# Optimization experiments

Hardware: AMD Instinct MI355X
Metric: run time of the kernel (lower is better)

The kernel has to match this reference:

```python
import jax, jax.numpy as jnp
import numpy as np

H = 1024   # hidden_size
E = 8      # num_experts
B = 8192   # num tokens


def setup_inputs() -> dict:
    key = jax.random.key(0)
    ks = jax.random.split(key, 7)
    s = 1.0 / np.sqrt(H)
    return {
        "inputs": jax.random.normal(ks[0], (B, H), jnp.float32),
        "Wr": jax.random.uniform(ks[1], (H, E), jnp.float32, -s, s),
        "br": jax.random.uniform(ks[2], (E,), jnp.float32, -s, s),
        "W1": jax.random.uniform(ks[3], (E, H, H), jnp.float32, -s, s),
        "b1": jax.random.uniform(ks[4], (E, H), jnp.float32, -s, s),
        "W2": jax.random.uniform(ks[5], (E, H, H), jnp.float32, -s, s),
        "b2": jax.random.uniform(ks[6], (E, H), jnp.float32, -s, s),
        "top_k": 2,
    }


def reference(inputs, Wr, br, W1, b1, W2, b2, top_k):
    # Router: softmax over experts
    logits = inputs @ Wr + br                      # [B, E]
    weights = jax.nn.softmax(logits, axis=-1)      # [B, E]

    # Top-k mask + renormalize (matches scatter_ mask semantics)
    top_values, top_indices = jax.lax.top_k(weights, top_k)  # [B, k]
    rows = jnp.arange(weights.shape[0])[:, None]
    mask = jnp.zeros_like(weights).at[rows, top_indices].set(1.0)
    masked = weights * mask
    masked = masked / (masked.sum(axis=-1, keepdims=True) + 1e-9)

    # Dense all-experts MLP: Linear -> GELU(exact) -> Linear
    h = jnp.einsum('bh,ehf->bef', inputs, W1) + b1            # [B, E, H]
    h = jax.nn.gelu(h, approximate=False)
    expert_out = jnp.einsum('bef,efh->beh', h, W2) + b2       # [B, E, H]

    combined = jnp.einsum('be,beh->bh', masked, expert_out)   # [B, H]
    return combined, weights
```

## Files before the change

kernel.cpp:

```cpp
#include <hip/hip_runtime.h>
#include <math.h>


#define HB 1024
#define NB 8192
#define NE 8
#define RTOK 16

#define BM 128
#define BN 128
#define BK 64

typedef unsigned short ushort_t;
typedef unsigned int u32;
typedef _Float16 f16;
typedef __attribute__((ext_vector_type(8))) _Float16 hfx8;
typedef __attribute__((ext_vector_type(4))) float f32x4;

__device__ __forceinline__ float gelu_exact(float x) {
  return 0.5f * x * (1.0f + erff(x * 0.70710678118654752440f));
}
__device__ __forceinline__ void gload16(const void* g, void* l) {
  __builtin_amdgcn_global_load_lds((const __attribute__((address_space(1))) u32*)g,
                                   (__attribute__((address_space(3))) u32*)l, 16, 0, 0);
}

__global__ void zero_cnt_kernel(int* cnt) {
  if (threadIdx.x < NE * 16) cnt[threadIdx.x] = 0;
}

__global__ __launch_bounds__(256) void zero_out_kernel(float4* __restrict__ out) {
  out[(size_t)blockIdx.x * 256 + threadIdx.x] = (float4){0.f, 0.f, 0.f, 0.f};
}

__global__ __launch_bounds__(256) void xsplit_kernel(
    const float* __restrict__ X, f16* __restrict__ Xh, f16* __restrict__ Xl)
{
  const size_t i = ((size_t)blockIdx.x * 256 + threadIdx.x) * 8;
  float4 a = *(const float4*)(X + i);
  float4 b = *(const float4*)(X + i + 4);
  float f[8] = {a.x, a.y, a.z, a.w, b.x, b.y, b.z, b.w};
  hfx8 h, l;
  #pragma unroll
  for (int q = 0; q < 8; ++q) {
    f16 hh = (f16)f[q];
    h[q] = hh;
    l[q] = (f16)(f[q] - (float)hh);
  }
  *(hfx8*)(Xh + i) = h;
  *(hfx8*)(Xl + i) = l;
}

__global__ __launch_bounds__(256) void wsplit_kernel(
    const float* __restrict__ W1, const float* __restrict__ W2,
    f16* __restrict__ T1h, f16* __restrict__ T2h)
{
  __shared__ float sT[32][33];
  const int e = blockIdx.z >> 1;
  const int which = blockIdx.z & 1;
  const float* W = (which ? W2 : W1) + ((size_t)e << 20);
  f16* Th = (which ? T2h : T1h) + ((size_t)e << 20);
  const int k0 = blockIdx.x << 5;
  const int n0 = blockIdx.y << 5;
  const int r = threadIdx.x >> 3;
  const int q = threadIdx.x & 7;
  float4 v = *(const float4*)(W + (size_t)(k0 + r) * HB + n0 + q * 4);
  sT[r][q*4+0] = v.x; sT[r][q*4+1] = v.y; sT[r][q*4+2] = v.z; sT[r][q*4+3] = v.w;
  __syncthreads();
  f16 hv[4];
  #pragma unroll
  for (int j = 0; j < 4; ++j) hv[j] = (f16)sT[q*4+j][r];
  const size_t off = (size_t)(n0 + r) * HB + k0 + q * 4;
  *(ushort4*)(Th + off) = *(ushort4*)hv;
}

__global__ __launch_bounds__(256) void router_kernel(
    const float* __restrict__ X, const float* __restrict__ Wr, const float* __restrict__ br,
    float* __restrict__ wout, int* __restrict__ cnt,
    int* __restrict__ list, float* __restrict__ wlist)
{
  __shared__ int   sCnt[NE];
  __shared__ int   sBase[NE];
  __shared__ int   sE[RTOK][2];
  __shared__ int   sOff[RTOK][2];
  __shared__ float sW[RTOK][2];

  const int tid = threadIdx.x;
  if (tid < NE) sCnt[tid] = 0;
  __syncthreads();

  const int wv = tid >> 6;
  const int lane = tid & 63;

  for (int i = 0; i < 4; ++i) {
    const int s = wv * 4 + i;
    const int t = blockIdx.x * RTOK + s;
    const float* xr = X + (size_t)t * HB;
    float p0=0,p1=0,p2=0,p3=0,p4=0,p5=0,p6=0,p7=0;
    for (int h0 = 0; h0 < HB; h0 += 64) {
      float xv = xr[h0 + lane];
      const float4 wa = *(const float4*)(Wr + (size_t)(h0 + lane) * NE);
      const float4 wb = *(const float4*)(Wr + (size_t)(h0 + lane) * NE + 4);
      p0 += xv * wa.x; p1 += xv * wa.y; p2 += xv * wa.z; p3 += xv * wa.w;
      p4 += xv * wb.x; p5 += xv * wb.y; p6 += xv * wb.z; p7 += xv * wb.w;
    }
    #pragma unroll
    for (int off = 1; off < 64; off <<= 1) {
      p0 += __shfl_xor(p0, off); p1 += __shfl_xor(p1, off);
      p2 += __shfl_xor(p2, off); p3 += __shfl_xor(p3, off);
      p4 += __shfl_xor(p4, off); p5 += __shfl_xor(p5, off);
      p6 += __shfl_xor(p6, off); p7 += __shfl_xor(p7, off);
    }
    if (lane == 0) {
      float w[8];
      w[0]=p0+br[0]; w[1]=p1+br[1]; w[2]=p2+br[2]; w[3]=p3+br[3];
      w[4]=p4+br[4]; w[5]=p5+br[5]; w[6]=p6+br[6]; w[7]=p7+br[7];
      float m = w[0];
      #pragma unroll
      for (int e = 1; e < 8; ++e) m = fmaxf(m, w[e]);
      float sm = 0.f;
      #pragma unroll
      for (int e = 0; e < 8; ++e) { w[e] = expf(w[e] - m); sm += w[e]; }
      const float inv = 1.f / sm;
      #pragma unroll
      for (int e = 0; e < 8; ++e) w[e] *= inv;
      float4 w03; w03.x=w[0]; w03.y=w[1]; w03.z=w[2]; w03.w=w[3];
      float4 w47; w47.x=w[4]; w47.y=w[5]; w47.z=w[6]; w47.w=w[7];
      *(float4*)(wout + (size_t)t * NE)     = w03;
      *(float4*)(wout + (size_t)t * NE + 4) = w47;
      int i0 = 0; float v0 = w[0];
      #pragma unroll
      for (int e = 1; e < 8; ++e) if (w[e] > v0) { v0 = w[e]; i0 = e; }
      int i1 = -1; float v1 = -1.f;
      #pragma unroll
      for (int e = 0; e < 8; ++e) if (e != i0 && w[e] > v1) { v1 = w[e]; i1 = e; }
      const float rn = 1.f / (v0 + v1 + 1e-9f);
      const int o0 = atomicAdd(&sCnt[i0], 1);
      const int o1 = atomicAdd(&sCnt[i1], 1);
      sE[s][0] = i0; sOff[s][0] = o0; sW[s][0] = v0 * rn;
      sE[s][1] = i1; sOff[s][1] = o1; sW[s][1] = v1 * rn;
    }
  }
  __syncthreads();
  if (tid < NE) sBase[tid] = atomicAdd(&cnt[tid * 16], sCnt[tid]);
  __syncthreads();
  if (tid < RTOK * 2) {
    const int s = tid >> 1, j = tid & 1;
    const int t = blockIdx.x * RTOK + s;
    const int e = sE[s][j];
    const int pos = sBase[e] + sOff[s][j];
    list[e * NB + pos]  = t * 2 + j;
    wlist[e * NB + pos] = sW[s][j];
  }
}

__global__ __launch_bounds__(256, 3) void gemm1_kernel(
    const f16* __restrict__ Xh, const f16* __restrict__ Xl,
    const f16* __restrict__ Wh,
    const float* __restrict__ b1, const int* __restrict__ cnt, const int* __restrict__ list,
    f16* __restrict__ H1h, f16* __restrict__ H1l)
{
  const int e = blockIdx.z;
  const int ne = cnt[e << 4];
  const int m0 = blockIdx.x * BM;
  if (m0 >= ne) return;
  const int n0 = blockIdx.y * BN;

  __shared__ f16 sAh[BM][BK], sAl[BM][BK], sB[BN][BK];
  __shared__ int sId[BM];

  const int tid = threadIdx.x;
  if (tid < BM) {
    int idx = m0 + tid;
    sId[tid] = (idx < ne) ? list[e * NB + idx] : -1;
  }
  __syncthreads();

  const int lane = tid & 63;
  const int w    = tid >> 6;
  const int rl    = lane >> 3;
  const int xslot = (lane & 7) ^ rl;

  const f16* srcAh[4]; const f16* srcAl[4]; const f16* srcB[4];
  f16* dAh[4]; f16* dAl[4]; f16* dB[4];
  #pragma unroll
  for (int c = 0; c < 4; ++c) {
    const int cr = w * 32 + c * 8 + rl;
    const int rid = sId[cr];
    const size_t tok = (size_t)(rid < 0 ? 0 : (rid >> 1));
    srcAh[c] = Xh + (tok << 10) + xslot * 8;
    srcAl[c] = Xl + (tok << 10) + xslot * 8;
    const size_t nr = (size_t)(n0 + cr);
    srcB[c]  = Wh + ((size_t)e << 20) + (nr << 10) + xslot * 8;
    dAh[c] = &sAh[w * 32 + c * 8][0];
    dAl[c] = &sAl[w * 32 + c * 8][0];
    dB[c]  = &sB [w * 32 + c * 8][0];
  }

  const int wr = w >> 1, wc = w & 1;
  const int lrow = lane & 15;
  const int sgrp = lane >> 4;
  const int xk   = lrow & 7;

  f32x4 acc[4][4];
  #pragma unroll
  for (int i = 0; i < 4; ++i)
    #pragma unroll
    for (int j = 0; j < 4; ++j) acc[i][j] = (f32x4){0.f, 0.f, 0.f, 0.f};

  for (int k0 = 0; k0 < HB; k0 += BK) {
    #pragma unroll
    for (int c = 0; c < 4; ++c) {
      gload16(srcAh[c] + k0, dAh[c]);
      gload16(srcAl[c] + k0, dAl[c]);
      gload16(srcB[c]  + k0, dB[c]);
    }
    __syncthreads();
    #pragma unroll
    for (int ks = 0; ks < 2; ++ks) {
      const int col = ((ks * 4 + sgrp) ^ xk) * 8;
      hfx8 ah[4], al[4], b[4];
      #pragma unroll
      for (int m = 0; m < 4; ++m) {
        const int row = wr * 64 + m * 16 + lrow;
        ah[m] = *(const hfx8*)&sAh[row][col];
        al[m] = *(const hfx8*)&sAl[row][col];
      }
      #pragma unroll
      for (int n = 0; n < 4; ++n) {
        const int row = wc * 64 + n * 16 + lrow;
        b[n] = *(const hfx8*)&sB[row][col];
      }
      #pragma unroll
      for (int m = 0; m < 4; ++m)
        #pragma unroll
        for (int n = 0; n < 4; ++n) {
          acc[m][n] = __builtin_amdgcn_mfma_f32_16x16x32_f16(ah[m], b[n], acc[m][n], 0, 0, 0);
          acc[m][n] = __builtin_amdgcn_mfma_f32_16x16x32_f16(al[m], b[n], acc[m][n], 0, 0, 0);
        }
    }
    __syncthreads();
  }

  const int rgrp = (lane >> 4) << 2;
  #pragma unroll
  for (int m = 0; m < 4; ++m)
    #pragma unroll
    for (int r = 0; r < 4; ++r) {
      const int row = wr * 64 + m * 16 + rgrp + r;
      const int orid = sId[row];
      if (orid < 0) continue;
      #pragma unroll
      for (int n = 0; n < 4; ++n) {
        const int col = n0 + wc * 64 + n * 16 + lrow;
        float v = acc[m][n][r] + b1[e * HB + col];
        v = gelu_exact(v);
        f16 h = (f16)v;
        H1h[(size_t)orid * HB + col] = h;
        H1l[(size_t)orid * HB + col] = (f16)(v - (float)h);
      }
    }
}

__global__ __launch_bounds__(256, 3) void gemm2_kernel(
    const f16* __restrict__ H1h, const f16* __restrict__ H1l,
    const f16* __restrict__ Wh,
    const float* __restrict__ b2, const int* __restrict__ cnt, const int* __restrict__ list,
    const float* __restrict__ wlist, float* __restrict__ out)
{
  const int e = blockIdx.z;
  const int ne = cnt[e << 4];
  const int m0 = blockIdx.x * BM;
  if (m0 >= ne) return;
  const int n0 = blockIdx.y * BN;

  __shared__ f16 sAh[BM][BK], sAl[BM][BK], sB[BN][BK];
  __shared__ int sId[BM];
  __shared__ float sWt[BM];

  const int tid = threadIdx.x;
  if (tid < BM) {
    int idx = m0 + tid;
    if (idx < ne) { sId[tid] = list[e * NB + idx]; sWt[tid] = wlist[e * NB + idx]; }
    else          { sId[tid] = -1;                 sWt[tid] = 0.f; }
  }
  __syncthreads();

  const int lane = tid & 63;
  const int w    = tid >> 6;
  const int rl    = lane >> 3;
  const int xslot = (lane & 7) ^ rl;

  const f16* srcAh[4]; const f16* srcAl[4]; const f16* srcB[4];
  f16* dAh[4]; f16* dAl[4]; f16* dB[4];
  #pragma unroll
  for (int c = 0; c < 4; ++c) {
    const int cr = w * 32 + c * 8 + rl;
    const int rid = sId[cr];
    const size_t rowid = (size_t)(rid < 0 ? 0 : rid);
    srcAh[c] = H1h + (rowid << 10) + xslot * 8;
    srcAl[c] = H1l + (rowid << 10) + xslot * 8;
    const size_t nr = (size_t)(n0 + cr);
    srcB[c]  = Wh + ((size_t)e << 20) + (nr << 10) + xslot * 8;
    dAh[c] = &sAh[w * 32 + c * 8][0];
    dAl[c] = &sAl[w * 32 + c * 8][0];
    dB[c]  = &sB [w * 32 + c * 8][0];
  }

  const int wr = w >> 1, wc = w & 1;
  const int lrow = lane & 15;
  const int sgrp = lane >> 4;
  const int xk   = lrow & 7;

  f32x4 acc[4][4];
  #pragma unroll
  for (int i = 0; i < 4; ++i)
    #pragma unroll
    for (int j = 0; j < 4; ++j) acc[i][j] = (f32x4){0.f, 0.f, 0.f, 0.f};

  for (int k0 = 0; k0 < HB; k0 += BK) {
    #pragma unroll
    for (int c = 0; c < 4; ++c) {
      gload16(srcAh[c] + k0, dAh[c]);
      gload16(srcAl[c] + k0, dAl[c]);
      gload16(srcB[c]  + k0, dB[c]);
    }
    __syncthreads();
    #pragma unroll
    for (int ks = 0; ks < 2; ++ks) {
      const int col = ((ks * 4 + sgrp) ^ xk) * 8;
      hfx8 ah[4], al[4], b[4];
      #pragma unroll
      for (int m = 0; m < 4; ++m) {
        const int row = wr * 64 + m * 16 + lrow;
        ah[m] = *(const hfx8*)&sAh[row][col];
        al[m] = *(const hfx8*)&sAl[row][col];
      }
      #pragma unroll
      for (int n = 0; n < 4; ++n) {
        const int row = wc * 64 + n * 16 + lrow;
        b[n] = *(const hfx8*)&sB[row][col];
      }
      #pragma unroll
      for (int m = 0; m < 4; ++m)
        #pragma unroll
        for (int n = 0; n < 4; ++n) {
          acc[m][n] = __builtin_amdgcn_mfma_f32_16x16x32_f16(ah[m], b[n], acc[m][n], 0, 0, 0);
          acc[m][n] = __builtin_amdgcn_mfma_f32_16x16x32_f16(al[m], b[n], acc[m][n], 0, 0, 0);
        }
    }
    __syncthreads();
  }

  const int rgrp = (lane >> 4) << 2;
  #pragma unroll
  for (int m = 0; m < 4; ++m)
    #pragma unroll
    for (int r = 0; r < 4; ++r) {
      const int row = wr * 64 + m * 16 + rgrp + r;
      const int orid = sId[row];
      if (orid < 0) continue;
      const float wrow = sWt[row];
      const size_t tok = (size_t)(orid >> 1);
      #pragma unroll
      for (int n = 0; n < 4; ++n) {
        const int col = n0 + wc * 64 + n * 16 + lrow;
        atomicAdd(&out[tok * HB + col], (acc[m][n][r] + b2[e * HB + col]) * wrow);
      }
    }
}

extern "C" void kernel_launch(void* const* d_in, const int* in_sizes, int n_in,
                              void* d_out, int out_size, void* d_ws, size_t ws_size,
                              hipStream_t stream) {
  const float* X  = (const float*)d_in[0];
  const float* Wr = (const float*)d_in[1];
  const float* br = (const float*)d_in[2];
  const float* W1 = (const float*)d_in[3];
  const float* b1 = (const float*)d_in[4];
  const float* W2 = (const float*)d_in[5];
  const float* b2 = (const float*)d_in[6];
  float* out = (float*)d_out;

  char* ws = (char*)d_ws;
  size_t o = 0;
  int*   cnt   = (int*)(ws + o);   o += 512;
  int*   list  = (int*)(ws + o);   o += (size_t)NE * NB * 4;
  float* wlist = (float*)(ws + o); o += (size_t)NE * NB * 4;
  f16*   T1h   = (f16*)(ws + o);   o += (size_t)NE * HB * HB * 2;
  f16*   T2h   = (f16*)(ws + o);   o += (size_t)NE * HB * HB * 2;
  f16*   H1h   = (f16*)(ws + o);   o += (size_t)NB * 2 * HB * 2;
  f16*   H1l   = (f16*)(ws + o);   o += (size_t)NB * 2 * HB * 2;
  f16*   Xh    = (f16*)(ws + o);   o += (size_t)NB * HB * 2;
  f16*   Xl    = (f16*)(ws + o);   o += (size_t)NB * HB * 2;

  zero_cnt_kernel<<<1, 128, 0, stream>>>(cnt);
  zero_out_kernel<<<NB * HB / 1024, 256, 0, stream>>>((float4*)out);
  xsplit_kernel<<<NB * HB / (8 * 256), 256, 0, stream>>>(X, Xh, Xl);
  wsplit_kernel<<<dim3(HB / 32, HB / 32, NE * 2), 256, 0, stream>>>(W1, W2, T1h, T2h);
  router_kernel<<<NB / RTOK, 256, 0, stream>>>(X, Wr, br, out + (size_t)NB * HB, cnt, list, wlist);
  gemm1_kernel<<<dim3(NB / BM, HB / BN, NE), 256, 0, stream>>>(Xh, Xl, T1h, b1, cnt, list, H1h, H1l);
  gemm2_kernel<<<dim3(NB / BM, HB / BN, NE), 256, 0, stream>>>(H1h, H1l, T2h, b2, cnt, list, wlist, out);
}
```

Measured before the change: 476.1 us.

## Enlarge GEMM tiles, double-buffer LDS, and replace atomics with combine pass

Both expert GEMMs move to 256x256 tiles with BK=32 and 512-thread blocks, and LDS tiles are double-buffered so the global-to-LDS loads of the next K slice overlap the MFMAs on the current one. The block index is remapped so the expert varies fastest, and wave priority is raised around the MFMA section. GEMM2 now writes per-slot weighted outputs to a scratch buffer that aliases the Xh/Xl region, instead of doing atomicAdd into the output. A separate combine kernel then sums the two slots per token, which also removes the output-zeroing kernel. The larger tiles increase register and LDS pressure and can waste more work on padded rows for experts with few tokens.

```diff
diff --git a/kernel.cpp b/kernel.cpp
--- a/kernel.cpp
+++ b/kernel.cpp
@@ -7,9 +7,9 @@
 #define NE 8
 #define RTOK 16
 
-#define BM 128
-#define BN 128
-#define BK 64
+#define BM 256
+#define BN 256
+#define BK 32
 
 typedef unsigned short ushort_t;
 typedef unsigned int u32;
@@ -27,10 +27,6 @@
 
 __global__ void zero_cnt_kernel(int* cnt) {
   if (threadIdx.x < NE * 16) cnt[threadIdx.x] = 0;
-}
-
-__global__ __launch_bounds__(256) void zero_out_kernel(float4* __restrict__ out) {
-  out[(size_t)blockIdx.x * 256 + threadIdx.x] = (float4){0.f, 0.f, 0.f, 0.f};
 }
 
 __global__ __launch_bounds__(256) void xsplit_kernel(
@@ -154,220 +150,200 @@
   }
 }
 
-__global__ __launch_bounds__(256, 3) void gemm1_kernel(
+#define STG(bf, k) do { \
+    gload16(pAh0 + (k), &sA[bf][0][w16][0]); \
+    gload16(pAh1 + (k), &sA[bf][0][128 + w16][0]); \
+    gload16(pAl0 + (k), &sA[bf][1][w16][0]); \
+    gload16(pAl1 + (k), &sA[bf][1][128 + w16][0]); \
+    gload16(pB0  + (k), &sB[bf][w16][0]); \
+    gload16(pB1  + (k), &sB[bf][128 + w16][0]); \
+  } while (0)
+
+#define MFMA_STEP(cur) do { \
+    hfx8 bfr[4]; \
+    _Pragma("unroll") \
+    for (int n = 0; n < 4; ++n) bfr[n] = *(const hfx8*)&sB[cur][wc * 64 + n * 16 + lrow][col]; \
+    __builtin_amdgcn_s_setprio(1); \
+    _Pragma("unroll") \
+    for (int m = 0; m < 8; ++m) { \
+      const hfx8 ah = *(const hfx8*)&sA[cur][0][wr * 128 + m * 16 + lrow][col]; \
+      const hfx8 al = *(const hfx8*)&sA[cur][1][wr * 128 + m * 16 + lrow][col]; \
+      _Pragma("unroll") \
+      for (int n = 0; n < 4; ++n) { \
+        acc[m][n] = __builtin_amdgcn_mfma_f32_16x16x32_f16(ah, bfr[n], acc[m][n], 0, 0, 0); \
+        acc[m][n] = __builtin_amdgcn_mfma_f32_16x16x32_f16(al, bfr[n], acc[m][n], 0, 0, 0); \
+      } \
+    } \
+    __builtin_amdgcn_s_setprio(0); \
+  } while (0)
+
+__global__ __launch_bounds__(512, 2) void gemm1_kernel(
     const f16* __restrict__ Xh, const f16* __restrict__ Xl,
     const f16* __restrict__ Wh,
     const float* __restrict__ b1, const int* __restrict__ cnt, const int* __restrict__ list,
     f16* __restrict__ H1h, f16* __restrict__ H1l)
 {
-  const int e = blockIdx.z;
-  const int ne = cnt[e << 4];
-  const int m0 = blockIdx.x * BM;
+  const int b  = blockIdx.x + (blockIdx.y << 5) + (blockIdx.z << 7);
+  const int ve = b & 7;
+  const int vn = (b >> 8) & 3;
+  const int vm = (b >> 3) & 31;
+  const int ne = cnt[ve << 4];
+  const int m0 = vm * BM;
   if (m0 >= ne) return;
-  const int n0 = blockIdx.y * BN;
-
-  __shared__ f16 sAh[BM][BK], sAl[BM][BK], sB[BN][BK];
+  const int n0 = vn * BN;
+
+  __shared__ f16 sA[2][2][BM][BK];
+  __shared__ f16 sB[2][BN][BK];
   __shared__ int sId[BM];
 
   const int tid = threadIdx.x;
   if (tid < BM) {
     int idx = m0 + tid;
-    sId[tid] = (idx < ne) ? list[e * NB + idx] : -1;
-  }
-  __syncthreads();
-
-  const int lane = tid & 63;
-  const int w    = tid >> 6;
-  const int rl    = lane >> 3;
-  const int xslot = (lane & 7) ^ rl;
-
-  const f16* srcAh[4]; const f16* srcAl[4]; const f16* srcB[4];
-  f16* dAh[4]; f16* dAl[4]; f16* dB[4];
-  #pragma unroll
-  for (int c = 0; c < 4; ++c) {
-    const int cr = w * 32 + c * 8 + rl;
-    const int rid = sId[cr];
-    const size_t tok = (size_t)(rid < 0 ? 0 : (rid >> 1));
-    srcAh[c] = Xh + (tok << 10) + xslot * 8;
-    srcAl[c] = Xl + (tok << 10) + xslot * 8;
-    const size_t nr = (size_t)(n0 + cr);
-    srcB[c]  = Wh + ((size_t)e << 20) + (nr << 10) + xslot * 8;
-    dAh[c] = &sAh[w * 32 + c * 8][0];
-    dAl[c] = &sAl[w * 32 + c * 8][0];
-    dB[c]  = &sB [w * 32 + c * 8][0];
-  }
-
-  const int wr = w >> 1, wc = w & 1;
-  const int lrow = lane & 15;
-  const int sgrp = lane >> 4;
-  const int xk   = lrow & 7;
-
-  f32x4 acc[4][4];
-  #pragma unroll
-  for (int i = 0; i < 4; ++i)
+    sId[tid] = (idx < ne) ? list[ve * NB + idx] : -1;
+  }
+  __syncthreads();
+
+  const int lr = tid >> 2;
+  const int sl = (((tid & 3) ^ ((lr >> 1) & 3)) << 3);
+  const int rid0 = sId[lr], rid1 = sId[128 + lr];
+  const f16* pAh0 = Xh + ((size_t)(rid0 < 0 ? 0 : (rid0 >> 1)) << 10) + sl;
+  const f16* pAh1 = Xh + ((size_t)(rid1 < 0 ? 0 : (rid1 >> 1)) << 10) + sl;
+  const f16* pAl0 = Xl + ((size_t)(rid0 < 0 ? 0 : (rid0 >> 1)) << 10) + sl;
+  const f16* pAl1 = Xl + ((size_t)(rid1 < 0 ? 0 : (rid1 >> 1)) << 10) + sl;
+  const f16* pB0  = Wh + ((size_t)ve << 20) + ((size_t)(n0 + lr) << 10) + sl;
+  const f16* pB1  = Wh + ((size_t)ve << 20) + ((size_t)(n0 + 128 + lr) << 10) + sl;
+  const int w16 = (tid >> 6) << 4;
+
+  const int lane = tid & 63, wid = tid >> 6;
+  const int wr = wid >> 2, wc = wid & 3;
+  const int lrow = lane & 15, sgrp = lane >> 4;
+  const int col = ((sgrp ^ ((lrow >> 1) & 3)) << 3);
+
+  f32x4 acc[8][4];
+  #pragma unroll
+  for (int i = 0; i < 8; ++i)
     #pragma unroll
     for (int j = 0; j < 4; ++j) acc[i][j] = (f32x4){0.f, 0.f, 0.f, 0.f};
 
-  for (int k0 = 0; k0 < HB; k0 += BK) {
-    #pragma unroll
-    for (int c = 0; c < 4; ++c) {
-      gload16(srcAh[c] + k0, dAh[c]);
-      gload16(srcAl[c] + k0, dAl[c]);
-      gload16(srcB[c]  + k0, dB[c]);
-    }
+  STG(0, 0);
+  __syncthreads();
+  int cur = 0;
+  for (int t = 0; t < 31; ++t) {
+    STG(cur ^ 1, (t + 1) * BK);
+    MFMA_STEP(cur);
     __syncthreads();
-    #pragma unroll
-    for (int ks = 0; ks < 2; ++ks) {
-      const int col = ((ks * 4 + sgrp) ^ xk) * 8;
-      hfx8 ah[4], al[4], b[4];
-      #pragma unroll
-      for (int m = 0; m < 4; ++m) {
-        const int row = wr * 64 + m * 16 + lrow;
-        ah[m] = *(const hfx8*)&sAh[row][col];
-        al[m] = *(const hfx8*)&sAl[row][col];
-      }
-      #pragma unroll
-      for (int n = 0; n < 4; ++n) {
-        const int row = wc * 64 + n * 16 + lrow;
-        b[n] = *(const hfx8*)&sB[row][col];
-      }
-      #pragma unroll
-      for (int m = 0; m < 4; ++m)
-        #pragma unroll
-        for (int n = 0; n < 4; ++n) {
-          acc[m][n] = __builtin_amdgcn_mfma_f32_16x16x32_f16(ah[m], b[n], acc[m][n], 0, 0, 0);
-          acc[m][n] = __builtin_amdgcn_mfma_f32_16x16x32_f16(al[m], b[n], acc[m][n], 0, 0, 0);
-        }
-    }
-    __syncthreads();
-  }
+    cur ^= 1;
+  }
+  MFMA_STEP(cur);
 
   const int rgrp = (lane >> 4) << 2;
   #pragma unroll
-  for (int m = 0; m < 4; ++m)
+  for (int m = 0; m < 8; ++m)
     #pragma unroll
     for (int r = 0; r < 4; ++r) {
-      const int row = wr * 64 + m * 16 + rgrp + r;
+      const int row = wr * 128 + m * 16 + rgrp + r;
       const int orid = sId[row];
       if (orid < 0) continue;
       #pragma unroll
       for (int n = 0; n < 4; ++n) {
-        const int col = n0 + wc * 64 + n * 16 + lrow;
-        float v = acc[m][n][r] + b1[e * HB + col];
+        const int c = n0 + wc * 64 + n * 16 + lrow;
+        float v = acc[m][n][r] + b1[ve * HB + c];
         v = gelu_exact(v);
         f16 h = (f16)v;
-        H1h[(size_t)orid * HB + col] = h;
-        H1l[(size_t)orid * HB + col] = (f16)(v - (float)h);
+        H1h[(size_t)orid * HB + c] = h;
+        H1l[(size_t)orid * HB + c] = (f16)(v - (float)h);
       }
     }
 }
 
-__global__ __launch_bounds__(256, 3) void gemm2_kernel(
+__global__ __launch_bounds__(512, 2) void gemm2_kernel(
     const f16* __restrict__ H1h, const f16* __restrict__ H1l,
     const f16* __restrict__ Wh,
     const float* __restrict__ b2, const int* __restrict__ cnt, const int* __restrict__ list,
-    const float* __restrict__ wlist, float* __restrict__ out)
-{
-  const int e = blockIdx.z;
-  const int ne = cnt[e << 4];
-  const int m0 = blockIdx.x * BM;
+    const float* __restrict__ wlist, float* __restrict__ OUTC)
+{
+  const int b  = blockIdx.x + (blockIdx.y << 5) + (blockIdx.z << 7);
+  const int ve = b & 7;
+  const int vn = (b >> 8) & 3;
+  const int vm = (b >> 3) & 31;
+  const int ne = cnt[ve << 4];
+  const int m0 = vm * BM;
   if (m0 >= ne) return;
-  const int n0 = blockIdx.y * BN;
-
-  __shared__ f16 sAh[BM][BK], sAl[BM][BK], sB[BN][BK];
+  const int n0 = vn * BN;
+
+  __shared__ f16 sA[2][2][BM][BK];
+  __shared__ f16 sB[2][BN][BK];
   __shared__ int sId[BM];
   __shared__ float sWt[BM];
 
   const int tid = threadIdx.x;
   if (tid < BM) {
     int idx = m0 + tid;
-    if (idx < ne) { sId[tid] = list[e * NB + idx]; sWt[tid] = wlist[e * NB + idx]; }
-    else          { sId[tid] = -1;                 sWt[tid] = 0.f; }
-  }
-  __syncthreads();
-
-  const int lane = tid & 63;
-  const int w    = tid >> 6;
-  const int rl    = lane >> 3;
-  const int xslot = (lane & 7) ^ rl;
-
-  const f16* srcAh[4]; const f16* srcAl[4]; const f16* srcB[4];
-  f16* dAh[4]; f16* dAl[4]; f16* dB[4];
-  #pragma unroll
-  for (int c = 0; c < 4; ++c) {
-    const int cr = w * 32 + c * 8 + rl;
-    const int rid = sId[cr];
-    const size_t rowid = (size_t)(rid < 0 ? 0 : rid);
-    srcAh[c] = H1h + (rowid << 10) + xslot * 8;
-    srcAl[c] = H1l + (rowid << 10) + xslot * 8;
-    const size_t nr = (size_t)(n0 + cr);
-    srcB[c]  = Wh + ((size_t)e << 20) + (nr << 10) + xslot * 8;
-    dAh[c] = &sAh[w * 32 + c * 8][0];
-    dAl[c] = &sAl[w * 32 + c * 8][0];
-    dB[c]  = &sB [w * 32 + c * 8][0];
-  }
-
-  const int wr = w >> 1, wc = w & 1;
-  const int lrow = lane & 15;
-  const int sgrp = lane >> 4;
-  const int xk   = lrow & 7;
-
-  f32x4 acc[4][4];
-  #pragma unroll
-  for (int i = 0; i < 4; ++i)
+    if (idx < ne) { sId[tid] = list[ve * NB + idx]; sWt[tid] = wlist[ve * NB + idx]; }
+    else          { sId[tid] = -1;                  sWt[tid] = 0.f; }
+  }
+  __syncthreads();
+
+  const int lr = tid >> 2;
+  const int sl = (((tid & 3) ^ ((lr >> 1) & 3)) << 3);
+  const int rid0 = sId[lr], rid1 = sId[128 + lr];
+  const f16* pAh0 = H1h + ((size_t)(rid0 < 0 ? 0 : rid0) << 10) + sl;
+  const f16* pAh1 = H1h + ((size_t)(rid1 < 0 ? 0 : rid1) << 10) + sl;
+  const f16* pAl0 = H1l + ((size_t)(rid0 < 0 ? 0 : rid0) << 10) + sl;
+  const f16* pAl1 = H1l + ((size_t)(rid1 < 0 ? 0 : rid1) << 10) + sl;
+  const f16* pB0  = Wh + ((size_t)ve << 20) + ((size_t)(n0 + lr) << 10) + sl;
+  const f16* pB1  = Wh + ((size_t)ve << 20) + ((size_t)(n0 + 128 + lr) << 10) + sl;
+  const int w16 = (tid >> 6) << 4;
+
+  const int lane = tid & 63, wid = tid >> 6;
+  const int wr = wid >> 2, wc = wid & 3;
+  const int lrow = lane & 15, sgrp = lane >> 4;
+  const int col = ((sgrp ^ ((lrow >> 1) & 3)) << 3);
+
+  f32x4 acc[8][4];
+  #pragma unroll
+  for (int i = 0; i < 8; ++i)
     #pragma unroll
     for (int j = 0; j < 4; ++j) acc[i][j] = (f32x4){0.f, 0.f, 0.f, 0.f};
 
-  for (int k0 = 0; k0 < HB; k0 += BK) {
-    #pragma unroll
-    for (int c = 0; c < 4; ++c) {
-      gload16(srcAh[c] + k0, dAh[c]);
-      gload16(srcAl[c] + k0, dAl[c]);
-      gload16(srcB[c]  + k0, dB[c]);
-    }
+  STG(0, 0);
+  __syncthreads();
+  int cur = 0;
+  for (int t = 0; t < 31; ++t) {
+    STG(cur ^ 1, (t + 1) * BK);
+    MFMA_STEP(cur);
     __syncthreads();
-    #pragma unroll
-    for (int ks = 0; ks < 2; ++ks) {
-      const int col = ((ks * 4 + sgrp) ^ xk) * 8;
-      hfx8 ah[4], al[4], b[4];
-      #pragma unroll
-      for (int m = 0; m < 4; ++m) {
-        const int row = wr * 64 + m * 16 + lrow;
-        ah[m] = *(const hfx8*)&sAh[row][col];
-        al[m] = *(const hfx8*)&sAl[row][col];
-      }
-      #pragma unroll
-      for (int n = 0; n < 4; ++n) {
-        const int row = wc * 64 + n * 16 + lrow;
-        b[n] = *(const hfx8*)&sB[row][col];
-      }
-      #pragma unroll
-      for (int m = 0; m < 4; ++m)
-        #pragma unroll
-        for (int n = 0; n < 4; ++n) {
-          acc[m][n] = __builtin_amdgcn_mfma_f32_16x16x32_f16(ah[m], b[n], acc[m][n], 0, 0, 0);
-          acc[m][n] = __builtin_amdgcn_mfma_f32_16x16x32_f16(al[m], b[n], acc[m][n], 0, 0, 0);
-        }
-    }
-    __syncthreads();
-  }
+    cur ^= 1;
+  }
+  MFMA_STEP(cur);
 
   const int rgrp = (lane >> 4) << 2;
   #pragma unroll
-  for (int m = 0; m < 4; ++m)
+  for (int m = 0; m < 8; ++m)
     #pragma unroll
     for (int r = 0; r < 4; ++r) {
-      const int row = wr * 64 + m * 16 + rgrp + r;
+      const int row = wr * 128 + m * 16 + rgrp + r;
       const int orid = sId[row];
       if (orid < 0) continue;
       const float wrow = sWt[row];
-      const size_t tok = (size_t)(orid >> 1);
       #pragma unroll
       for (int n = 0; n < 4; ++n) {
-        const int col = n0 + wc * 64 + n * 16 + lrow;
-        atomicAdd(&out[tok * HB + col], (acc[m][n][r] + b2[e * HB + col]) * wrow);
+        const int c = n0 + wc * 64 + n * 16 + lrow;
+        OUTC[(size_t)orid * HB + c] = (acc[m][n][r] + b2[ve * HB + c]) * wrow;
       }
     }
+}
+
+__global__ __launch_bounds__(256) void combine_kernel(
+    const float* __restrict__ OUTC, float* __restrict__ out)
+{
+  const int i = blockIdx.x * 256 + threadIdx.x;
+  const int t = i >> 8;
+  const int c4 = i & 255;
+  const float4 a = *((const float4*)(OUTC + ((size_t)t << 11)) + c4);
+  const float4 b = *((const float4*)(OUTC + ((size_t)t << 11) + HB) + c4);
+  float4 o; o.x = a.x + b.x; o.y = a.y + b.y; o.z = a.z + b.z; o.w = a.w + b.w;
+  *((float4*)out + i) = o;
 }
 
 extern "C" void kernel_launch(void* const* d_in, const int* in_sizes, int n_in,
@@ -391,14 +367,16 @@
   f16*   T2h   = (f16*)(ws + o);   o += (size_t)NE * HB * HB * 2;
   f16*   H1h   = (f16*)(ws + o);   o += (size_t)NB * 2 * HB * 2;
   f16*   H1l   = (f16*)(ws + o);   o += (size_t)NB * 2 * HB * 2;
-  f16*   Xh    = (f16*)(ws + o);   o += (size_t)NB * HB * 2;
-  f16*   Xl    = (f16*)(ws + o);   o += (size_t)NB * HB * 2;
+  char*  region = ws + o;          o += (size_t)NB * 2 * HB * 4;
+  f16*   Xh = (f16*)region;
+  f16*   Xl = (f16*)(region + (size_t)NB * HB * 2);
+  float* OUTC = (float*)region;
 
   zero_cnt_kernel<<<1, 128, 0, stream>>>(cnt);
-  zero_out_kernel<<<NB * HB / 1024, 256, 0, stream>>>((float4*)out);
   xsplit_kernel<<<NB * HB / (8 * 256), 256, 0, stream>>>(X, Xh, Xl);
   wsplit_kernel<<<dim3(HB / 32, HB / 32, NE * 2), 256, 0, stream>>>(W1, W2, T1h, T2h);
   router_kernel<<<NB / RTOK, 256, 0, stream>>>(X, Wr, br, out + (size_t)NB * HB, cnt, list, wlist);
-  gemm1_kernel<<<dim3(NB / BM, HB / BN, NE), 256, 0, stream>>>(Xh, Xl, T1h, b1, cnt, list, H1h, H1l);
-  gemm2_kernel<<<dim3(NB / BM, HB / BN, NE), 256, 0, stream>>>(H1h, H1l, T2h, b2, cnt, list, wlist, out);
-}
+  gemm1_kernel<<<dim3(NB / BM, HB / BN, NE), 512, 0, stream>>>(Xh, Xl, T1h, b1, cnt, list, H1h, H1l);
+  gemm2_kernel<<<dim3(NB / BM, HB / BN, NE), 512, 0, stream>>>(H1h, H1l, T2h, b2, cnt, list, wlist, OUTC);
+  combine_kernel<<<NB * HB / 1024, 256, 0, stream>>>(OUTC, out);
+}
```

Result: slower. 494.2 us (+3.8%).
